# Optimization experiments

Measured on AMD Instinct MI355X. Metric: run time of the kernel, lower is better.

Reference implementation:

```python
import jax, jax.numpy as jnp
import numpy as np

# Model dims (rexgen/WLN canonical hyperparameters)
B, N, MAXNB, NBONDS = 16, 100, 10, 120
AF, BF, H, BIN = 82, 6, 300, 11
DEPTH, K = 3, 80


def setup_inputs() -> dict:
    key = jax.random.key(0)
    ks = jax.random.split(key, 24)
    f32 = jnp.float32
    inp = {}
    inp["fatoms"] = jax.random.normal(ks[0], (B, N, AF), f32)
    inp["fbonds"] = jax.random.normal(ks[1], (B, NBONDS, BF), f32)
    inp["atom_nb"] = jax.random.randint(ks[2], (B, N, MAXNB), 0, N)
    inp["bond_nb"] = jax.random.randint(ks[3], (B, N, MAXNB), 0, NBONDS)
    inp["num_nbs"] = jnp.full((B, N), MAXNB, jnp.int32)
    inp["n_atoms"] = jnp.full((B,), N, jnp.int32)
    inp["binary_feats"] = jax.random.normal(ks[4], (B, N, N, BIN), f32)
    inp["mask_neis"] = (jax.random.uniform(ks[5], (B, N, MAXNB, 1)) > 0.2).astype(f32)
    inp["mask_atoms"] = jnp.ones((B, N, 1), f32)
    # sparse_idx enumerates all (sample, atom_i, atom_j) pairs in row-major order
    sb = jnp.repeat(jnp.arange(B), N * N)
    si = jnp.tile(jnp.repeat(jnp.arange(N), N), B)
    sj = jnp.tile(jnp.arange(N), B * N)
    inp["sparse_idx"] = jnp.stack([sb, si, sj], axis=1).astype(jnp.int32)

    def w(k, shape):
        return jax.random.normal(k, shape, f32) * 0.1

    # WLNet params
    inp["W_atom"] = w(ks[6], (AF, H))
    inp["W_nei_atom"] = w(ks[7], (H, H))
    inp["W_nei_bond"] = w(ks[8], (BF, H))
    inp["W_self"] = w(ks[9], (H, H))
    inp["W_U2"] = w(ks[10], (H + BF, H)); inp["b_U2"] = jnp.zeros((H,), f32)
    inp["W_U1"] = w(ks[11], (2 * H, H)); inp["b_U1"] = jnp.zeros((H,), f32)
    # Attention params
    inp["W_att_local"] = w(ks[12], (H, H))
    inp["W_att_bin"] = w(ks[13], (BIN, H)); inp["b_att"] = jnp.zeros((H,), f32)
    inp["W_att_score"] = w(ks[14], (H, 1)); inp["b_att_score"] = jnp.zeros((1,), f32)
    # ReactivityScoring params
    inp["W_pl"] = w(ks[15], (H, H))
    inp["W_pg"] = w(ks[16], (H, H))
    inp["W_pb"] = w(ks[17], (BIN, H)); inp["b_p"] = jnp.zeros((H,), f32)
    inp["W_out"] = w(ks[18], (H, 1)); inp["b_out"] = jnp.zeros((1,), f32)
    return inp


def _pair_scores(fatoms, fbonds, binary_feats, mask_neis, mask_atoms,
                 W_atom, W_nei_atom, W_nei_bond, W_self, W_U2, b_U2, W_U1, b_U1,
                 W_att_local, W_att_bin, b_att, W_att_score, b_att_score,
                 W_pl, W_pg, W_pb, b_p, W_out, b_out,
                 atom_nb, bond_nb, sparse_idx):
    bidx = jnp.arange(B)[:, None, None]
    # --- WLNet graph convolution ---
    h = jax.nn.relu(fatoms @ W_atom)                       # [B,N,H]
    local = h
    for _ in range(DEPTH):
        fnei_atom = h[bidx, atom_nb]                       # [B,N,MAXNB,H]
        fnei_bond = fbonds[bidx, bond_nb]                  # [B,N,MAXNB,BF]
        h_nei = (fnei_atom @ W_nei_atom) * (fnei_bond @ W_nei_bond)
        f_nei = (h_nei * mask_neis).sum(axis=2)            # [B,N,H]
        f_self = h @ W_self
        local = f_nei * f_self * mask_atoms                # kernel output
        nei_label = jax.nn.relu(jnp.concatenate([fnei_atom, fnei_bond], -1) @ W_U2 + b_U2)
        nei_label = (nei_label * mask_neis).sum(axis=2)
        h = jax.nn.relu(jnp.concatenate([h, nei_label], -1) @ W_U1 + b_U1)
    # --- Global attention over atom pairs ---
    pair = local[:, :, None, :] + local[:, None, :, :]     # [B,N,N,H]
    att_h = jax.nn.relu(pair @ W_att_local + binary_feats @ W_att_bin + b_att)
    att_s = jax.nn.sigmoid(att_h @ W_att_score + b_att_score)  # [B,N,N,1]
    ctx = jnp.einsum('bij,bjh->bih', att_s[..., 0], local)     # [B,N,H]
    # --- Gather sparse pairs and score reactivity ---
    sb, si, sj = sparse_idx[:, 0], sparse_idx[:, 1], sparse_idx[:, 2]
    local_pair = local[sb, si] + local[sb, sj]             # [P,H]
    global_pair = ctx[sb, si] + ctx[sb, sj]                # [P,H]
    bin_pair = binary_feats[sb, si, sj]                    # [P,BIN]
    hid = jax.nn.relu(local_pair @ W_pl + global_pair @ W_pg + bin_pair @ W_pb + b_p)
    return hid @ W_out + b_out                             # [P,1]


def reference(fatoms, fbonds, atom_nb, bond_nb, num_nbs, n_atoms, binary_feats,
              mask_neis, mask_atoms, sparse_idx,
              W_atom, W_nei_atom, W_nei_bond, W_self, W_U2, b_U2, W_U1, b_U1,
              W_att_local, W_att_bin, b_att, W_att_score, b_att_score,
              W_pl, W_pg, W_pb, b_p, W_out, b_out):
    pair_scores = _pair_scores(fatoms, fbonds, binary_feats, mask_neis, mask_atoms,
                               W_atom, W_nei_atom, W_nei_bond, W_self, W_U2, b_U2, W_U1, b_U1,
                               W_att_local, W_att_bin, b_att, W_att_score, b_att_score,
                               W_pl, W_pg, W_pb, b_p, W_out, b_out,
                               atom_nb, bond_nb, sparse_idx)
    # Segmented top-k: sparse_idx rows are grouped & ordered by sample with
    # exactly N*N pairs each, so per-sample flatten == reshape to [B, N*N].
    _, topks = jax.lax.top_k(pair_scores.reshape(B, N * N), K)  # indices, matching torch.topk[1]
    return pair_scores, topks
```

## Files before the change

### kernel.cpp

```cpp
#include <hip/hip_runtime.h>
#include <hip/hip_bf16.h>
#include <math.h>

#define BB 16
#define NN 100
#define MAXNB 10
#define NBONDS 120
#define AF 82
#define BF 6
#define HH 300
#define BIN 11
#define DEPTH 3
#define KTOP 80

typedef __attribute__((ext_vector_type(8))) short short8;
typedef __attribute__((ext_vector_type(4))) float floatx4;

__device__ __forceinline__ unsigned short f2bf(float f) {
    unsigned int u = __float_as_uint(f);
    unsigned int r = (u + 0x7FFFu + ((u >> 16) & 1u)) >> 16;
    return (unsigned short)r;
}
__device__ __forceinline__ float bf2f(unsigned short h) {
    return __uint_as_float(((unsigned int)h) << 16);
}

#define O_WATOM 0
#define O_WNB   29184
#define O_U2B   38912
#define O_WNA   48640
#define O_U2A   145920
#define O_WSELF 243200
#define O_U1A   340480
#define O_U1B   437760
#define O_WATT  535040
#define O_WPL   632320
#define O_WPG   729600

__global__ __launch_bounds__(256) void k_prep(
    const float* __restrict__ s0, const float* __restrict__ s1,
    const float* __restrict__ s2, const float* __restrict__ s3,
    const float* __restrict__ s4, const float* __restrict__ s5,
    const float* __restrict__ s6, const float* __restrict__ s7,
    const float* __restrict__ s8, const float* __restrict__ s9,
    const float* __restrict__ s10,
    unsigned short* __restrict__ WTh, unsigned short* __restrict__ WTl,
    const float* __restrict__ fatoms, const float* __restrict__ fbonds,
    unsigned short* __restrict__ fatomsbf, unsigned short* __restrict__ fbondsbf,
    const float* __restrict__ bin, unsigned short* __restrict__ BINBF,
    const float* __restrict__ Wbin0, const float* __restrict__ Wbin1,
    unsigned short* __restrict__ WBF0, unsigned short* __restrict__ WBF1)
{
    const int z = blockIdx.z;
    if (z == 11) {
        int idx = blockIdx.x * 256 + threadIdx.x;
        if (idx < 1600 * 96) {
            int r = idx / 96, c = idx - r * 96;
            float f = (c < AF) ? fatoms[r * AF + c] : 0.f;
            unsigned short hb = f2bf(f);
            fatomsbf[r * 192 + c]      = hb;
            fatomsbf[r * 192 + 96 + c] = f2bf(f - bf2f(hb));
        } else {
            int i2 = idx - 1600 * 96;
            if (i2 < 1920 * 32) {
                int r = i2 / 32, c = i2 - r * 32;
                float f = (c < BF) ? fbonds[r * BF + c] : 0.f;
                unsigned short hb = f2bf(f);
                fbondsbf[r * 64 + c]      = hb;
                fbondsbf[r * 64 + 32 + c] = f2bf(f - bf2f(hb));
            }
        }
        return;
    }
    if (z == 12) {
        const int bx = blockIdx.x;
        if (bx < 625) {
            int p = bx * 256 + threadIdx.x;
            if (p < BB * NN * NN) {
                const float* src = bin + (size_t)p * BIN;
                unsigned short tmp[16];
#pragma unroll
                for (int k = 0; k < BIN; k++) tmp[k] = f2bf(src[k]);
#pragma unroll
                for (int k = BIN; k < 16; k++) tmp[k] = 0;
                *(uint4*)(BINBF + (size_t)p * 16) = *(uint4*)tmp;
                *(uint4*)(BINBF + (size_t)p * 16 + 8) = *(uint4*)(tmp + 8);
            }
        } else if (bx < 663) {
            int zb = bx - 625;
            const float* src = (zb >= 19) ? Wbin1 : Wbin0;
            unsigned short* dst = (zb >= 19) ? WBF1 : WBF0;
            int idx = (zb % 19) * 256 + threadIdx.x;
            int jj = idx & 7;
            int koct = (idx >> 3) & 1;
            int n = (idx >> 4) & 15;
            int ch = idx >> 8;
            int k = koct * 8 + jj;
            int h = ch * 16 + n;
            float f = (k < BIN && h < 300) ? src[k * 300 + h] : 0.f;
            dst[idx] = f2bf(f);
        }
        return;
    }
    const float* src; int K, kc, off;
    switch (z) {
        case 0:  src = s0;  K = AF;  kc = 3;  off = O_WATOM; break;
        case 1:  src = s1;  K = BF;  kc = 1;  off = O_WNB;   break;
        case 2:  src = s2;  K = BF;  kc = 1;  off = O_U2B;   break;
        case 3:  src = s3;  K = HH;  kc = 10; off = O_WNA;   break;
        case 4:  src = s4;  K = HH;  kc = 10; off = O_U2A;   break;
        case 5:  src = s5;  K = HH;  kc = 10; off = O_WSELF; break;
        case 6:  src = s6;  K = HH;  kc = 10; off = O_U1A;   break;
        case 7:  src = s7;  K = HH;  kc = 10; off = O_U1B;   break;
        case 8:  src = s8;  K = HH;  kc = 10; off = O_WATT;  break;
        case 9:  src = s9;  K = HH;  kc = 10; off = O_WPL;   break;
        default: src = s10; K = HH;  kc = 10; off = O_WPG;   break;
    }
    const int lim = 9728 * kc;
    int i = blockIdx.x * 256 + threadIdx.x;
    if (i < lim) {
        int jj = i & 7;
        int lane = (i >> 3) & 63;
        int rem = i >> 9;
        int kci = rem % kc;
        int ct = rem / kc;
        int k = kci * 32 + (lane >> 4) * 8 + jj;
        int col = ct * 16 + (lane & 15);
        float f = (k < K && col < 300) ? src[k * 300 + col] : 0.f;
        unsigned short hb = f2bf(f);
        WTh[off + i] = hb;
        WTl[off + i] = f2bf(f - bf2f(hb));
    }
}

__device__ __forceinline__ void gemm_core(
    const unsigned short* __restrict__ A, int lda, int kc, int M,
    const unsigned short* __restrict__ wthB, const unsigned short* __restrict__ wtlB,
    float* __restrict__ C, int ldc,
    const float* __restrict__ bias,
    const float* __restrict__ Add, int ldAdd, int addOff,
    int act, unsigned short* __restrict__ Cbf,
    int row0, int gcolBase)
{
    __shared__ unsigned short sa[16 * 648];
    if (row0 >= M) return;
    const int tid = threadIdx.x;
    const int lane = tid & 63;
    const int wid = tid >> 6;
    const int sR = kc * 64 + 8;

    {
        const uint4* Ag = (const uint4*)A;
        uint4* sa4 = (uint4*)sa;
        const int q4 = kc * 8;
        const int lda4 = lda >> 3;
        const int sR4 = q4 + 1;
        for (int i = tid; i < 16 * q4; i += 256) {
            int r = i / q4, q = i - r * q4;
            sa4[r * sR4 + q] = Ag[(size_t)(row0 + r) * lda4 + q];
        }
    }
    __syncthreads();

    const int ct = blockIdx.y * 4 + wid;
    if (ct >= 19) return;

    const int m = lane & 15;
    const int rq = lane >> 4;
    const int koct8 = rq * 8;
    const unsigned short* wth = wthB + (size_t)ct * kc * 512;
    const unsigned short* wtl = wtlB + (size_t)ct * kc * 512;

    floatx4 acc = {0.f, 0.f, 0.f, 0.f};
    for (int kci = 0; kci < kc; kci++) {
        short8 ah = *(const short8*)(sa + m * sR + kci * 32 + koct8);
        short8 al = *(const short8*)(sa + m * sR + kc * 32 + kci * 32 + koct8);
        short8 wh = *(const short8*)(wth + (kci * 64 + lane) * 8);
        short8 wl = *(const short8*)(wtl + (kci * 64 + lane) * 8);
        acc = __builtin_amdgcn_mfma_f32_16x16x32_bf16(ah, wl, acc, 0, 0, 0);
        acc = __builtin_amdgcn_mfma_f32_16x16x32_bf16(al, wh, acc, 0, 0, 0);
        acc = __builtin_amdgcn_mfma_f32_16x16x32_bf16(ah, wh, acc, 0, 0, 0);
    }

    const int col = ct * 16 + m;
    if (col < 300) {
        const float bv = bias ? bias[col] : 0.f;
        const int gcol = gcolBase + col;
#pragma unroll
        for (int r = 0; r < 4; r++) {
            const int grow = row0 + rq * 4 + r;
            float v = acc[r] + bv;
            if (Add) v += Add[(size_t)grow * ldAdd + addOff + col];
            if (act) v = fmaxf(v, 0.f);
            if (C) C[(size_t)grow * ldc + gcol] = v;
            if (Cbf) {
                unsigned short hb = f2bf(v);
                Cbf[(size_t)grow * 640 + col]       = hb;
                Cbf[(size_t)grow * 640 + 320 + col] = f2bf(v - bf2f(hb));
            }
        }
    }
}

__global__ __launch_bounds__(256) void k_gemm_mfma(
    const unsigned short* __restrict__ A, int lda, int kc, int M,
    const unsigned short* __restrict__ WTh, const unsigned short* __restrict__ WTl,
    int wtStride,
    float* __restrict__ C, int ldc,
    const float* __restrict__ bias,
    const float* __restrict__ Add, int ldAdd, int addOff,
    int act, unsigned short* __restrict__ Cbf)
{
    const int widx = blockIdx.z;
    gemm_core(A, lda, kc, M,
              WTh + (size_t)widx * wtStride, WTl + (size_t)widx * wtStride,
              C, ldc, bias, Add, ldAdd, addOff, act, Cbf,
              blockIdx.x * 16, widx * 300);
}

__global__ __launch_bounds__(256) void k_gemm_first(
    const unsigned short* __restrict__ fatomsbf,
    const unsigned short* __restrict__ fbondsbf,
    const unsigned short* __restrict__ WTh, const unsigned short* __restrict__ WTl,
    unsigned short* __restrict__ hbf, float* __restrict__ FBout)
{
    const int z = blockIdx.z;
    if (z == 0) {
        gemm_core(fatomsbf, 192, 3, 1600,
                  WTh + O_WATOM, WTl + O_WATOM,
                  nullptr, 0, nullptr, nullptr, 0, 0, 1, hbf,
                  blockIdx.x * 16, 0);
    } else {
        const int w = z - 1;
        gemm_core(fbondsbf, 64, 1, 1920,
                  WTh + O_WNB + w * 9728, WTl + O_WNB + w * 9728,
                  FBout, 600, nullptr, nullptr, 0, 0, 0, nullptr,
                  blockIdx.x * 16, w * 300);
    }
}

__global__ __launch_bounds__(320) void k_neighbor(
    const float* __restrict__ HW, const float* __restrict__ FB,
    const int* __restrict__ atom_nb, const int* __restrict__ bond_nb,
    const float* __restrict__ mask_neis, const float* __restrict__ mask_atoms,
    const float* __restrict__ b_U2,
    unsigned short* __restrict__ localbf, unsigned short* __restrict__ nlbf)
{
    __shared__ int   sAn[4][MAXNB];
    __shared__ int   sBd[4][MAXNB];
    __shared__ float sM[4][MAXNB];
    const int tx = threadIdx.x;
    const int ty = threadIdx.y;
    const int bx = blockIdx.x;
    const int bn0 = ((bx & 15) * 25 + (bx >> 4)) * 4;
    const int flat = ty * 80 + tx;

    if (flat < 40)        sAn[flat / 10][flat % 10] = atom_nb[(bn0 + flat / 10) * MAXNB + flat % 10];
    else if (flat < 80)  { int f = flat - 40; sBd[f / 10][f % 10] = bond_nb[(bn0 + f / 10) * MAXNB + f % 10]; }
    else if (flat < 120) { int f = flat - 80; sM[f / 10][f % 10]  = mask_neis[(bn0 + f / 10) * MAXNB + f % 10]; }
    __syncthreads();

    if (tx >= 75) return;
    const int bn = bn0 + ty;
    const int b = bn / NN;
    const int h4 = tx;

    const float4* HW4 = (const float4*)HW;
    const float4* FB4 = (const float4*)FB;
    const float4 bu = ((const float4*)b_U2)[h4];

    float4 fnei = make_float4(0.f,0.f,0.f,0.f);
    float4 nls  = fnei;
#pragma unroll
    for (int k = 0; k < MAXNB; k++) {
        const int an = sAn[ty][k];
        const int bd = sBd[ty][k];
        const float m = sM[ty][k];
        const float4* hr = HW4 + (size_t)(b * NN + an) * 300;
        const float4* fr = FB4 + (size_t)(b * NBONDS + bd) * 150;
        float4 ha = hr[h4];
        float4 hu = hr[75 + h4];
        float4 fa = fr[h4];
        float4 fu = fr[75 + h4];
        fnei.x = fmaf(m, ha.x * fa.x, fnei.x);
        fnei.y = fmaf(m, ha.y * fa.y, fnei.y);
        fnei.z = fmaf(m, ha.z * fa.z, fnei.z);
        fnei.w = fmaf(m, ha.w * fa.w, fnei.w);
        float ux = hu.x + fu.x + bu.x;
        float uy = hu.y + fu.y + bu.y;
        float uz = hu.z + fu.z + bu.z;
        float uw = hu.w + fu.w + bu.w;
        nls.x = fmaf(m, fmaxf(ux, 0.f), nls.x);
        nls.y = fmaf(m, fmaxf(uy, 0.f), nls.y);
        nls.z = fmaf(m, fmaxf(uz, 0.f), nls.z);
        nls.w = fmaf(m, fmaxf(uw, 0.f), nls.w);
    }
    const float ma = mask_atoms[bn];
    const float4 sf = HW4[(size_t)bn * 300 + 150 + h4];
    float lv[4], nv[4];
    lv[0] = fnei.x * sf.x * ma; lv[1] = fnei.y * sf.y * ma;
    lv[2] = fnei.z * sf.z * ma; lv[3] = fnei.w * sf.w * ma;
    nv[0] = nls.x; nv[1] = nls.y; nv[2] = nls.z; nv[3] = nls.w;

    ushort4 lh, ll, nh, nl2;
    unsigned short* lhp = (unsigned short*)&lh;
    unsigned short* llp = (unsigned short*)&ll;
    unsigned short* nhp = (unsigned short*)&nh;
    unsigned short* nlp = (unsigned short*)&nl2;
#pragma unroll
    for (int c = 0; c < 4; c++) {
        unsigned short hb = f2bf(lv[c]);
        lhp[c] = hb; llp[c] = f2bf(lv[c] - bf2f(hb));
        unsigned short nb = f2bf(nv[c]);
        nhp[c] = nb; nlp[c] = f2bf(nv[c] - bf2f(nb));
    }
    *(ushort4*)(localbf + (size_t)bn * 640 + h4 * 4)       = lh;
    *(ushort4*)(localbf + (size_t)bn * 640 + 320 + h4 * 4) = ll;
    *(ushort4*)(nlbf    + (size_t)bn * 640 + h4 * 4)       = nh;
    *(ushort4*)(nlbf    + (size_t)bn * 640 + 320 + h4 * 4) = nl2;
}

__global__ __launch_bounds__(256) void k_pair(
    const float* __restrict__ R, int ldr,
    const unsigned short* __restrict__ BINBF,
    const unsigned short* __restrict__ WBF,
    const float* __restrict__ bvec,
    const float* __restrict__ Wscore, const float* __restrict__ bscore,
    float* __restrict__ outp, int mode)
{
    __shared__ float sLi[16 * 308];
    __shared__ float sLj[16 * 308];

    const int b  = blockIdx.x;
    const int i0 = blockIdx.y * 16;
    const int j0 = blockIdx.z * 16;
    const int tid = threadIdx.x;
    const int lane = tid & 63;
    const int wid = tid >> 6;

    for (int idx = tid; idx < 16 * 308; idx += 256) {
        int r = idx / 308;
        int c = idx - r * 308;
        float vi = 0.f, vj = 0.f;
        if (c < 300) {
            if (i0 + r < NN) vi = R[(size_t)(b * NN + i0 + r) * ldr + c] + bvec[c];
            if (j0 + r < NN) vj = R[(size_t)(b * NN + j0 + r) * ldr + c];
        }
        sLi[idx] = vi;
        sLj[idx] = vj;
    }

    const int m = lane & 15;
    const int koct = lane >> 4;
    short8 afrag[4];
#pragma unroll
    for (int g = 0; g < 4; g++) {
        int ii = i0 + wid * 4 + g; if (ii > NN - 1) ii = NN - 1;
        int jj2 = j0 + m;          if (jj2 > NN - 1) jj2 = NN - 1;
        const size_t pidx = (size_t)((b * NN + ii) * NN + jj2);
        afrag[g] = *(const short8*)(BINBF + pidx * 16 + (koct & 1) * 8);
        if (koct >= 2) afrag[g] = short8{0,0,0,0,0,0,0,0};
    }
    __syncthreads();

    const int n = lane & 15;
    const int rquad = lane >> 4;
    const floatx4 zero = {0.f, 0.f, 0.f, 0.f};
    float su[4][4];
#pragma unroll
    for (int g = 0; g < 4; g++)
#pragma unroll
        for (int r = 0; r < 4; r++) su[g][r] = 0.f;

    for (int ch = 0; ch < 19; ch++) {
        const int h0 = ch * 16;
        short8 bfrag = {0,0,0,0,0,0,0,0};
        if (lane < 32)
            bfrag = *(const short8*)(WBF + ch * 256 + (n * 2 + koct) * 8);
        float wsv = 0.f;
        if (h0 + n < 300) wsv = Wscore[h0 + n];
#pragma unroll
        for (int g = 0; g < 4; g++) {
            floatx4 P = __builtin_amdgcn_mfma_f32_16x16x32_bf16(
                afrag[g], bfrag, zero, 0, 0, 0);
            const float liv = sLi[(wid * 4 + g) * 308 + h0 + n];
#pragma unroll
            for (int r = 0; r < 4; r++) {
                const float ljv = sLj[(rquad * 4 + r) * 308 + h0 + n];
                float u = P[r] + liv + ljv;
                su[g][r] = fmaf(fmaxf(u, 0.f), wsv, su[g][r]);
            }
        }
    }

    const float bs = bscore[0];
#pragma unroll
    for (int g = 0; g < 4; g++) {
#pragma unroll
        for (int r = 0; r < 4; r++) {
            float v = su[g][r];
            v += __shfl_xor(v, 1);
            v += __shfl_xor(v, 2);
            v += __shfl_xor(v, 4);
            v += __shfl_xor(v, 8);
            if (n == 0) {
                const int i = i0 + wid * 4 + g;
                const int j = j0 + rquad * 4 + r;
                if (i < NN && j < NN) {
                    float s = v + bs;
                    outp[(size_t)(b * NN + i) * NN + j] =
                        (mode == 0) ? (1.f / (1.f + expf(-s))) : s;
                }
            }
        }
    }
}

__global__ __launch_bounds__(320) void k_ctx(
    const float* __restrict__ att, const unsigned short* __restrict__ localbf,
    unsigned short* __restrict__ ctxbf)
{
    const int bx = blockIdx.x;
    const int b = bx & 15;
    const int i0 = (bx >> 4) * 4;
    const int tid = threadIdx.x;
    __shared__ float sa[4 * NN];
    for (int idx = tid; idx < 4 * NN; idx += 320) {
        int ii = idx / NN, j = idx - ii * NN;
        sa[idx] = att[(size_t)(b * NN + i0 + ii) * NN + j];
    }
    __syncthreads();
    if (tid < HH) {
        float acc0 = 0.f, acc1 = 0.f, acc2 = 0.f, acc3 = 0.f;
        for (int j = 0; j < NN; j++) {
            const unsigned short* lr = localbf + (size_t)(b * NN + j) * 640;
            float lv = bf2f(lr[tid]) + bf2f(lr[320 + tid]);
            acc0 = fmaf(sa[j], lv, acc0);
            acc1 = fmaf(sa[NN + j], lv, acc1);
            acc2 = fmaf(sa[2 * NN + j], lv, acc2);
            acc3 = fmaf(sa[3 * NN + j], lv, acc3);
        }
        float vals[4] = {acc0, acc1, acc2, acc3};
#pragma unroll
        for (int k = 0; k < 4; k++) {
            unsigned short hb = f2bf(vals[k]);
            ctxbf[(size_t)(b * NN + i0 + k) * 640 + tid]       = hb;
            ctxbf[(size_t)(b * NN + i0 + k) * 640 + 320 + tid] = f2bf(vals[k] - bf2f(hb));
        }
    }
}

__global__ __launch_bounds__(1024) void k_topk(
    const float* __restrict__ scores, float* __restrict__ topk_out)
{
    const int b = blockIdx.x;
    const int tid = threadIdx.x;
    const int wid = tid >> 6;
    const int lane = tid & 63;
    const float* sc = scores + (size_t)b * (NN * NN);

    __shared__ unsigned int skey[NN * NN];
    __shared__ unsigned int whist[16 * 256];
    __shared__ unsigned int hist[256];
    __shared__ unsigned int candU[KTOP];
    __shared__ int candI[KTOP];
    __shared__ int cntG;
    __shared__ int curMin;
    __shared__ unsigned int sh_pref, sh_mask;
    __shared__ int sh_kRem;
    __shared__ int sh_last;

    for (int idx = tid; idx < NN * NN; idx += 1024) {
        unsigned int u = __float_as_uint(sc[idx]);
        u = (u & 0x80000000u) ? ~u : (u | 0x80000000u);
        skey[idx] = u;
    }
    if (tid == 0) {
        sh_pref = 0u; sh_mask = 0u; sh_kRem = KTOP; cntG = 0; sh_last = -1;
    }
    __syncthreads();

    for (int pass = 0; pass < 4; pass++) {
        const int shift = 24 - 8 * pass;
        unsigned int* wh = whist + (wid << 8);
        wh[lane] = 0u; wh[lane + 64] = 0u; wh[lane + 128] = 0u; wh[lane + 192] = 0u;
        __syncthreads();
        const unsigned int pref = sh_pref, mask = sh_mask;
        for (int idx = tid; idx < NN * NN; idx += 1024) {
            unsigned int u = skey[idx];
            if ((u & mask) == pref)
                atomicAdd(&wh[(u >> shift) & 255u], 1u);
        }
        __syncthreads();
        if (tid < 256) {
            unsigned int s = 0u;
#pragma unroll
            for (int w = 0; w < 16; w++) s += whist[(w << 8) | tid];
            hist[tid] = s;
        }
        __syncthreads();
        if (wid == 0) {
            unsigned int h0 = hist[lane * 4 + 0];
            unsigned int h1 = hist[lane * 4 + 1];
            unsigned int h2 = hist[lane * 4 + 2];
            unsigned int h3 = hist[lane * 4 + 3];
            unsigned int own = h0 + h1 + h2 + h3;
            unsigned int suf = own;
#pragma unroll
            for (int off = 1; off < 64; off <<= 1) {
                unsigned int v = __shfl_down(suf, off);
                if (lane + off < 64) suf += v;
            }
            const int k = sh_kRem;
            const unsigned int above = suf - own;
            if (above < (unsigned int)k && suf >= (unsigned int)k) {
                unsigned int c = above, hb; int bsel;
                c += h3;
                if ((int)c >= k) { bsel = lane * 4 + 3; hb = h3; }
                else { c += h2;
                    if ((int)c >= k) { bsel = lane * 4 + 2; hb = h2; }
                    else { c += h1;
                        if ((int)c >= k) { bsel = lane * 4 + 1; hb = h1; }
                        else { c += h0; bsel = lane * 4; hb = h0; } } }
                sh_kRem = k - (int)(c - hb);
                sh_pref = pref | ((unsigned int)bsel << shift);
                sh_mask = mask | (0xFFu << shift);
            }
        }
        __syncthreads();
    }
    const unsigned int T = sh_pref;

    for (int idx = tid; idx < NN * NN; idx += 1024) {
        unsigned int u = skey[idx];
        if (u > T) {
            int pos = atomicAdd(&cntG, 1);
            candU[pos] = u;
            candI[pos] = idx;
        }
    }
    __syncthreads();
    const int needE = KTOP - cntG;

    for (int e = 0; e < needE; e++) {
        if (tid == 0) curMin = 0x7fffffff;
        __syncthreads();
        const int last = sh_last;
        for (int idx = tid; idx < NN * NN; idx += 1024) {
            if (skey[idx] == T && idx > last)
                atomicMin(&curMin, idx);
        }
        __syncthreads();
        if (tid == 0) {
            candU[cntG + e] = T;
            candI[cntG + e] = curMin;
            sh_last = curMin;
        }
        __syncthreads();
    }

    if (tid < KTOP) {
        const unsigned int mu = candU[tid];
        const int mi = candI[tid];
        int rank = 0;
        for (int o = 0; o < KTOP; o++) {
            unsigned int ou = candU[o];
            int oi = candI[o];
            if (ou > mu || (ou == mu && oi < mi)) rank++;
        }
        topk_out[b * KTOP + rank] = (float)mi;
    }
}

extern "C" void kernel_launch(void* const* d_in, const int* in_sizes, int n_in,
                              void* d_out, int out_size, void* d_ws, size_t ws_size,
                              hipStream_t stream) {
    const float* fatoms       = (const float*)d_in[0];
    const float* fbonds       = (const float*)d_in[1];
    const int*   atom_nb      = (const int*)d_in[2];
    const int*   bond_nb      = (const int*)d_in[3];
    const float* binary_feats = (const float*)d_in[6];
    const float* mask_neis    = (const float*)d_in[7];
    const float* mask_atoms   = (const float*)d_in[8];
    const float* W_atom       = (const float*)d_in[10];
    const float* W_nei_atom   = (const float*)d_in[11];
    const float* W_nei_bond   = (const float*)d_in[12];
    const float* W_self       = (const float*)d_in[13];
    const float* W_U2         = (const float*)d_in[14];
    const float* b_U2         = (const float*)d_in[15];
    const float* W_U1         = (const float*)d_in[16];
    const float* b_U1         = (const float*)d_in[17];
    const float* W_att_local  = (const float*)d_in[18];
    const float* W_att_bin    = (const float*)d_in[19];
    const float* b_att        = (const float*)d_in[20];
    const float* W_att_score  = (const float*)d_in[21];
    const float* b_att_score  = (const float*)d_in[22];
    const float* W_pl         = (const float*)d_in[23];
    const float* W_pg         = (const float*)d_in[24];
    const float* W_pb         = (const float*)d_in[25];
    const float* b_p          = (const float*)d_in[26];
    const float* W_out        = (const float*)d_in[27];
    const float* b_out        = (const float*)d_in[28];

    float* ws = (float*)d_ws;
    float* HW  = ws;
    float* FB  = HW + 1920000;
    float* LL  = FB + 1152000;
    float* LPG = LL + 960000;
    float* att = LPG + 480000;
    unsigned short* S0       = (unsigned short*)(ws + 4672000);
    unsigned short* hbf      = S0;
    unsigned short* nlbf     = S0 + 1024000;
    unsigned short* localbf  = S0 + 2048000;
    unsigned short* WTh      = S0 + 3072000;
    unsigned short* WTl      = S0 + 3898880;
    unsigned short* ctxbf    = S0 + 4725760;
    unsigned short* BINBF    = S0 + 5749760;
    unsigned short* WBF_att  = S0 + 8309760;
    unsigned short* WBF_fin  = S0 + 8314624;
    unsigned short* fatomsbf = S0 + 8319488;
    unsigned short* fbondsbf = S0 + 8626688;

    float* out = (float*)d_out;
    float* topk_out = out + (size_t)BB * NN * NN;

    k_prep<<<dim3(840, 1, 13), 256, 0, stream>>>(
        W_atom, W_nei_bond, W_U2 + 300 * 300, W_nei_atom, W_U2, W_self,
        W_U1, W_U1 + 300 * 300, W_att_local, W_pl, W_pg, WTh, WTl,
        fatoms, fbonds, fatomsbf, fbondsbf,
        binary_feats, BINBF, W_att_bin, W_pb, WBF_att, WBF_fin);

    k_gemm_first<<<dim3(120, 5, 3), 256, 0, stream>>>(
        fatomsbf, fbondsbf, WTh, WTl, hbf, FB);

    for (int d = 0; d < DEPTH; d++) {
        int nW = (d == DEPTH - 1) ? 3 : 4;
        k_gemm_mfma<<<dim3(104, 5, nW), 256, 0, stream>>>(
            hbf, 640, 10, 1600, WTh + O_WNA, WTl + O_WNA, 97280,
            HW, 1200, nullptr, nullptr, 0, 0, 0, nullptr);
        k_neighbor<<<dim3(400), dim3(80, 4), 0, stream>>>(
            HW, FB, atom_nb, bond_nb, mask_neis, mask_atoms, b_U2,
            localbf, nlbf);
        if (d < DEPTH - 1) {
            k_gemm_mfma<<<dim3(104, 5, 1), 256, 0, stream>>>(
                nlbf, 640, 10, 1600, WTh + O_U1B, WTl + O_U1B, 0,
                nullptr, 0, b_U1, HW, 1200, 900, 1, hbf);
        }
    }

    k_gemm_mfma<<<dim3(104, 5, 2), 256, 0, stream>>>(
        localbf, 640, 10, 1600, WTh + O_WATT, WTl + O_WATT, 97280,
        LL, 600, nullptr, nullptr, 0, 0, 0, nullptr);

    k_pair<<<dim3(16, 7, 7), 256, 0, stream>>>(
        LL, 600, BINBF, WBF_att, b_att, W_att_score, b_att_score,
        att, 0);

    k_ctx<<<dim3(BB * 25), 320, 0, stream>>>(att, localbf, ctxbf);

    k_gemm_mfma<<<dim3(104, 5, 1), 256, 0, stream>>>(
        ctxbf, 640, 10, 1600, WTh + O_WPG, WTl + O_WPG, 0,
        LPG, 300, nullptr, LL, 600, 300, 0, nullptr);

    k_pair<<<dim3(16, 7, 7), 256, 0, stream>>>(
        LPG, 300, BINBF, WBF_fin, b_p, W_out, b_out,
        out, 1);

    k_topk<<<dim3(BB), 1024, 0, stream>>>(out, topk_out);
}
```

Measured before the change: 297.0 us.

## Fuse attention-context reduction with the global-pair projection GEMM

The attention-weighted context computation and the following W_pg projection GEMM are merged into one kernel. The context rows are kept in shared memory as split bf16 hi/lo pairs, and MFMA is applied directly to them, with the LL residual added at the end. This removes one launch and the ctxbf round trip through global memory. In exchange the grid is much smaller (112 blocks instead of 400 plus 520), which may underuse the GPU. Each thread also holds 16 accumulators and reads localbf serially, so the per-block work is longer.

```diff
diff --git a/kernel.cpp b/kernel.cpp
--- a/kernel.cpp
+++ b/kernel.cpp
@@ -416,36 +416,85 @@
     }
 }
 
-__global__ __launch_bounds__(320) void k_ctx(
+__global__ __launch_bounds__(256) void k_ctxlpg(
     const float* __restrict__ att, const unsigned short* __restrict__ localbf,
-    unsigned short* __restrict__ ctxbf)
+    const unsigned short* __restrict__ WThPG, const unsigned short* __restrict__ WTlPG,
+    const float* __restrict__ LL, float* __restrict__ LPG)
 {
-    const int bx = blockIdx.x;
-    const int b = bx & 15;
-    const int i0 = (bx >> 4) * 4;
+    __shared__ float sAtt[16 * 100];
+    __shared__ unsigned short sa[16 * 648];
+    const int b  = blockIdx.x;
+    const int i0 = blockIdx.y * 16;
     const int tid = threadIdx.x;
-    __shared__ float sa[4 * NN];
-    for (int idx = tid; idx < 4 * NN; idx += 320) {
-        int ii = idx / NN, j = idx - ii * NN;
-        sa[idx] = att[(size_t)(b * NN + i0 + ii) * NN + j];
+    const int lane = tid & 63;
+    const int wid = tid >> 6;
+
+    for (int idx = tid; idx < 1600; idx += 256) {
+        int ii = idx / 100, j = idx - ii * 100;
+        float v = 0.f;
+        if (i0 + ii < NN) v = att[(size_t)(b * NN + i0 + ii) * NN + j];
+        sAtt[idx] = v;
     }
     __syncthreads();
-    if (tid < HH) {
-        float acc0 = 0.f, acc1 = 0.f, acc2 = 0.f, acc3 = 0.f;
-        for (int j = 0; j < NN; j++) {
-            const unsigned short* lr = localbf + (size_t)(b * NN + j) * 640;
-            float lv = bf2f(lr[tid]) + bf2f(lr[320 + tid]);
-            acc0 = fmaf(sa[j], lv, acc0);
-            acc1 = fmaf(sa[NN + j], lv, acc1);
-            acc2 = fmaf(sa[2 * NN + j], lv, acc2);
-            acc3 = fmaf(sa[3 * NN + j], lv, acc3);
-        }
-        float vals[4] = {acc0, acc1, acc2, acc3};
-#pragma unroll
-        for (int k = 0; k < 4; k++) {
-            unsigned short hb = f2bf(vals[k]);
-            ctxbf[(size_t)(b * NN + i0 + k) * 640 + tid]       = hb;
-            ctxbf[(size_t)(b * NN + i0 + k) * 640 + 320 + tid] = f2bf(vals[k] - bf2f(hb));
+
+#pragma unroll
+    for (int hbase = 0; hbase < 2; hbase++) {
+        const int h = tid + hbase * 256;
+        if (h < 300) {
+            float acc[16];
+#pragma unroll
+            for (int i = 0; i < 16; i++) acc[i] = 0.f;
+            for (int j = 0; j < NN; j++) {
+                const unsigned short* lr = localbf + (size_t)(b * NN + j) * 640;
+                float lv = bf2f(lr[h]) + bf2f(lr[320 + h]);
+#pragma unroll
+                for (int i = 0; i < 16; i++)
+                    acc[i] = fmaf(sAtt[i * 100 + j], lv, acc[i]);
+            }
+#pragma unroll
+            for (int i = 0; i < 16; i++) {
+                unsigned short hb = f2bf(acc[i]);
+                sa[i * 648 + h] = hb;
+                sa[i * 648 + 320 + h] = f2bf(acc[i] - bf2f(hb));
+            }
+        }
+    }
+    if (tid < 20) {
+#pragma unroll
+        for (int i = 0; i < 16; i++) {
+            sa[i * 648 + 300 + tid] = 0;
+            sa[i * 648 + 320 + 300 + tid] = 0;
+        }
+    }
+    __syncthreads();
+
+    const int m = lane & 15;
+    const int rq = lane >> 4;
+    const int koct8 = rq * 8;
+    for (int ct = wid; ct < 19; ct += 4) {
+        const unsigned short* wth = WThPG + (size_t)ct * 10 * 512;
+        const unsigned short* wtl = WTlPG + (size_t)ct * 10 * 512;
+        floatx4 acc = {0.f, 0.f, 0.f, 0.f};
+        for (int kci = 0; kci < 10; kci++) {
+            short8 ah = *(const short8*)(sa + m * 648 + kci * 32 + koct8);
+            short8 al = *(const short8*)(sa + m * 648 + 320 + kci * 32 + koct8);
+            short8 wh = *(const short8*)(wth + (kci * 64 + lane) * 8);
+            short8 wl = *(const short8*)(wtl + (kci * 64 + lane) * 8);
+            acc = __builtin_amdgcn_mfma_f32_16x16x32_bf16(ah, wl, acc, 0, 0, 0);
+            acc = __builtin_amdgcn_mfma_f32_16x16x32_bf16(al, wh, acc, 0, 0, 0);
+            acc = __builtin_amdgcn_mfma_f32_16x16x32_bf16(ah, wh, acc, 0, 0, 0);
+        }
+        const int col = ct * 16 + m;
+        if (col < 300) {
+#pragma unroll
+            for (int r = 0; r < 4; r++) {
+                const int i = i0 + rq * 4 + r;
+                if (i < NN) {
+                    const int grow = b * NN + i;
+                    LPG[(size_t)grow * 300 + col] =
+                        acc[r] + LL[(size_t)grow * 600 + 300 + col];
+                }
+            }
         }
     }
 }
@@ -614,12 +663,11 @@
     unsigned short* localbf  = S0 + 2048000;
     unsigned short* WTh      = S0 + 3072000;
     unsigned short* WTl      = S0 + 3898880;
-    unsigned short* ctxbf    = S0 + 4725760;
-    unsigned short* BINBF    = S0 + 5749760;
-    unsigned short* WBF_att  = S0 + 8309760;
-    unsigned short* WBF_fin  = S0 + 8314624;
-    unsigned short* fatomsbf = S0 + 8319488;
-    unsigned short* fbondsbf = S0 + 8626688;
+    unsigned short* BINBF    = S0 + 4725760;
+    unsigned short* WBF_att  = S0 + 7285760;
+    unsigned short* WBF_fin  = S0 + 7290624;
+    unsigned short* fatomsbf = S0 + 7295488;
+    unsigned short* fbondsbf = S0 + 7602688;
 
     float* out = (float*)d_out;
     float* topk_out = out + (size_t)BB * NN * NN;
@@ -656,11 +704,8 @@
         LL, 600, BINBF, WBF_att, b_att, W_att_score, b_att_score,
         att, 0);
 
-    k_ctx<<<dim3(BB * 25), 320, 0, stream>>>(att, localbf, ctxbf);
-
-    k_gemm_mfma<<<dim3(104, 5, 1), 256, 0, stream>>>(
-        ctxbf, 640, 10, 1600, WTh + O_WPG, WTl + O_WPG, 0,
-        LPG, 300, nullptr, LL, 600, 300, 0, nullptr);
+    k_ctxlpg<<<dim3(16, 7), 256, 0, stream>>>(
+        att, localbf, WTh + O_WPG, WTl + O_WPG, LL, LPG);
 
     k_pair<<<dim3(16, 7, 7), 256, 0, stream>>>(
         LPG, 300, BINBF, WBF_fin, b_p, W_out, b_out,
```

Result: slower. 329.4 us (+10.9%).
